# Kernel tuning notes

Hardware: AMD Instinct MI355X
Metric: run time of the kernel (lower is better)

The kernel has to match this reference:

```python
import jax, jax.numpy as jnp
import numpy as np

B, N, M, L, H = 32, 4096, 256, 128, 4
GAMMA = 2.0


def setup_inputs() -> dict:
    key = jax.random.key(0)
    kx, km, kv, ku, kw = jax.random.split(key, 5)
    x = jax.random.normal(kx, (B, N, M), dtype=jnp.float32)
    masks = (jax.random.uniform(km, (B, N)) > 0.3).astype(jnp.float32)
    # VarianceScaling(scale=0.1, fan_in, uniform) ~ small init; exact dist doesn't affect math
    V = jax.random.normal(kv, (H, M, L), dtype=jnp.float32) * 0.02
    U = jax.random.normal(ku, (H, M, L), dtype=jnp.float32) * 0.02
    w = jax.random.normal(kw, (H, L, 1), dtype=jnp.float32) * 0.05
    return {"x": x, "masks": masks, "V": V, "U": U, "w": w}


def reference(x, masks, V, U, w):
    # x: [B,N,M], masks: [B,N], V/U: [H,M,L], w: [H,L,1]
    m = masks[:, None, :, None]  # [B,1,N,1] broadcast over heads
    gated = jnp.tanh(jnp.einsum('bnm,hml->bhnl', x, V)) * jax.nn.sigmoid(
        jnp.einsum('bnm,hml->bhnl', x, U))          # [B,H,N,L]
    logits = jnp.einsum('bhnl,hl->bhn', gated, w[..., 0])[..., None]  # [B,H,N,1]
    a = m * logits                                   # masked logits (as in original)
    a = m * jnp.exp(a)                               # masked exp
    a = a / jnp.sum(a, axis=2, keepdims=True)        # softmax over instances
    ag = a ** GAMMA
    a = ag / jnp.sum(ag, axis=2, keepdims=True)      # gamma-power renorm
    emb = jnp.einsum('bhnk,bnm->bhm', a, x)          # weighted sum; k is the trailing 1
    emb = emb.reshape(B, H * M)                      # concat heads along axis=1
    att = jnp.transpose(a, (1, 0, 2, 3))             # [H,B,N,1] (per-head attention list)
    return (att, emb)
```

## Files before the change

### kernel.cpp

```cpp
#include <hip/hip_runtime.h>
#include <hip/hip_bf16.h>
#include <stdint.h>

#define B_ 32
#define N_ 4096
#define M_ 256
#define L_ 128
#define H_ 4
#define BN_ (B_ * N_)

typedef __bf16 bf16x8 __attribute__((ext_vector_type(8)));
typedef float  f32x4  __attribute__((ext_vector_type(4)));

__device__ __forceinline__ unsigned short f2bf(float f) {
    unsigned int u = __float_as_uint(f);
    u += 0x7fffu + ((u >> 16) & 1u);
    return (unsigned short)(u >> 16);
}
__device__ __forceinline__ unsigned int pack2(float lo, float hi) {
    return (unsigned int)f2bf(lo) | ((unsigned int)f2bf(hi) << 16);
}

__device__ __forceinline__ void gload16(const void* g, void* l) {
    __builtin_amdgcn_global_load_lds(
        (const __attribute__((address_space(1))) unsigned int*)g,
        (__attribute__((address_space(3))) unsigned int*)l, 16, 0, 0);
}


__global__ void prep_x(const float* __restrict__ x, unsigned short* __restrict__ xb) {
    const int blk  = blockIdx.x;
    const int tile = blk >> 2, ks = blk & 3;
    const int i    = threadIdx.x;
    const int kk   = (i & 7) * 8;
    const int tl   = kk >> 5;
    const int kl   = kk & 31;
    char* dst = (char*)xb + ((size_t)tile * 8 + ks * 2 + tl) * 8192;
#pragma unroll
    for (int rep = 0; rep < 4; ++rep) {
        int row = rep * 32 + (i >> 3);
        const float* gx = x + (size_t)(tile * 128 + row) * M_ + ks * 64 + kk;
        float4 a = *(const float4*)gx;
        float4 b = *(const float4*)(gx + 4);
        uint4 o;
        o.x = pack2(a.x, a.y); o.y = pack2(a.z, a.w);
        o.z = pack2(b.x, b.y); o.w = pack2(b.z, b.w);
        int byte = (row * 64 + kl * 2) ^ ((row & 6) << 3);
        *(uint4*)(dst + byte) = o;
    }
}

__global__ void prep_vu_img(const float* __restrict__ V, const float* __restrict__ U,
                            unsigned short* __restrict__ vu) {
    __shared__ float slab[64][129];
    const int b   = blockIdx.x;
    const int mat = b & 1, ks = (b >> 1) & 3, h = b >> 3;
    const float* src = (mat ? U : V) + ((size_t)h * M_ + ks * 64) * L_;
    const int tid = threadIdx.x;
#pragma unroll
    for (int rep = 0; rep < 32; ++rep) {
        int idx = rep * 256 + tid;
        slab[idx >> 7][idx & 127] = src[(size_t)(idx >> 7) * L_ + (idx & 127)];
    }
    __syncthreads();
#pragma unroll
    for (int rep = 0; rep < 4; ++rep) {
        int cidx = rep * 256 + tid;
        int l  = cidx >> 3;
        int kk = (cidx & 7) * 8;
        uint4 o;
        o.x = pack2(slab[kk + 0][l], slab[kk + 1][l]);
        o.y = pack2(slab[kk + 2][l], slab[kk + 3][l]);
        o.z = pack2(slab[kk + 4][l], slab[kk + 5][l]);
        o.w = pack2(slab[kk + 6][l], slab[kk + 7][l]);
        int tl = kk >> 5, kl = kk & 31;
        char* dst = (char*)vu + (((size_t)(h * 8 + ks * 2 + tl)) * 2 + mat) * 8192;
        int byte = (l * 64 + kl * 2) ^ ((l & 6) << 3);
        *(uint4*)(dst + byte) = o;
    }
}

__global__ __launch_bounds__(256, 2)
void gemm_fast3(const unsigned short* __restrict__ xb,
                const unsigned short* __restrict__ vu,
                const float* __restrict__ w,
                float* __restrict__ logits) {
    __shared__ __align__(16) unsigned short xs[3][4096];
    __shared__ __align__(16) unsigned short vs[3][4096];
    __shared__ __align__(16) unsigned short us[3][4096];

    const int orig    = blockIdx.x;
    const int logical = (orig & 7) * 512 + (orig >> 3);
    const int tile    = logical >> 2;
    const int h       = logical & 3;

    const int tid  = threadIdx.x;
    const int lane = tid & 63;
    const int wv   = tid >> 6;
    const int g    = lane >> 4;
    const int c    = lane & 15;

    f32x4 accV[2][8], accU[2][8];
#pragma unroll
    for (int rf = 0; rf < 2; ++rf)
#pragma unroll
        for (int cf = 0; cf < 8; ++cf) {
            accV[rf][cf] = (f32x4){0.f, 0.f, 0.f, 0.f};
            accU[rf][cf] = (f32x4){0.f, 0.f, 0.f, 0.f};
        }

    const int soff = wv * 2048;

    const char* gxs = (const char*)xb + (size_t)tile * 65536 + soff + lane * 16;
    const char* gvs = (const char*)vu + (size_t)h * 131072 + soff + lane * 16;
    const char* gus = gvs + 8192;

    int ar = wv * 32 + c;
    const int aoff0 = (ar * 64 + g * 16) ^ ((ar & 6) << 3);
    const int aoff1 = ((ar + 16) * 64 + g * 16) ^ (((ar + 16) & 6) << 3);
    int boff[8];
#pragma unroll
    for (int cf = 0; cf < 8; ++cf) {
        int l = cf * 16 + c;
        boff[cf] = (l * 64 + g * 16) ^ ((l & 6) << 3);
    }

#define STAGE(t, bufi) do {                                          \
        const char* _gx = gxs + (t) * 8192;                          \
        const char* _gv = gvs + (t) * 16384;                         \
        const char* _gu = gus + (t) * 16384;                         \
        gload16(_gx,        (char*)xs[bufi] + soff);                 \
        gload16(_gx + 1024, (char*)xs[bufi] + soff + 1024);          \
        gload16(_gv,        (char*)vs[bufi] + soff);                 \
        gload16(_gv + 1024, (char*)vs[bufi] + soff + 1024);          \
        gload16(_gu,        (char*)us[bufi] + soff);                 \
        gload16(_gu + 1024, (char*)us[bufi] + soff + 1024);          \
    } while (0)

    STAGE(0, 0);
    STAGE(1, 1);

#pragma unroll
    for (int t = 0; t < 8; ++t) {
        if (t < 7) asm volatile("s_waitcnt vmcnt(6)" ::: "memory");
        else       asm volatile("s_waitcnt vmcnt(0)" ::: "memory");
        __builtin_amdgcn_s_barrier();
        __builtin_amdgcn_sched_barrier(0);

        if (t < 6) STAGE(t + 2, (t + 2) % 3);

        const int buf = t % 3;
        const char* xbuf = (const char*)xs[buf];
        const char* vbuf = (const char*)vs[buf];
        const char* ubuf = (const char*)us[buf];

        bf16x8 a0 = *(const bf16x8*)(xbuf + aoff0);
        bf16x8 a1 = *(const bf16x8*)(xbuf + aoff1);
#pragma unroll
        for (int cf = 0; cf < 8; ++cf) {
            bf16x8 bv = *(const bf16x8*)(vbuf + boff[cf]);
            bf16x8 bu = *(const bf16x8*)(ubuf + boff[cf]);
            accV[0][cf] = __builtin_amdgcn_mfma_f32_16x16x32_bf16(a0, bv, accV[0][cf], 0, 0, 0);
            accV[1][cf] = __builtin_amdgcn_mfma_f32_16x16x32_bf16(a1, bv, accV[1][cf], 0, 0, 0);
            accU[0][cf] = __builtin_amdgcn_mfma_f32_16x16x32_bf16(a0, bu, accU[0][cf], 0, 0, 0);
            accU[1][cf] = __builtin_amdgcn_mfma_f32_16x16x32_bf16(a1, bu, accU[1][cf], 0, 0, 0);
        }
    }
#undef STAGE

    const float* wrow = w + h * L_;
#pragma unroll
    for (int rf = 0; rf < 2; ++rf) {
        float plog[4] = {0.f, 0.f, 0.f, 0.f};
#pragma unroll
        for (int cf = 0; cf < 8; ++cf) {
            float wvv = wrow[cf * 16 + c];
#pragma unroll
            for (int i = 0; i < 4; ++i) {
                float vv = accV[rf][cf][i];
                float uu = accU[rf][cf][i];
                vv = fminf(fmaxf(vv, -20.f), 20.f);
                float A = __expf(2.f * vv);
                float E = __expf(fminf(-uu, 30.f));
                float gg = __fdividef(A - 1.f, (A + 1.f) * (1.f + E));
                plog[i] += gg * wvv;
            }
        }
#pragma unroll
        for (int i = 0; i < 4; ++i) {
            float v = plog[i];
            v += __shfl_xor(v, 1);
            v += __shfl_xor(v, 2);
            v += __shfl_xor(v, 4);
            v += __shfl_xor(v, 8);
            if (c == 0) {
                int rowflat = tile * 128 + wv * 32 + rf * 16 + g * 4 + i;
                int b = rowflat >> 12;
                int n = rowflat & (N_ - 1);
                logits[((size_t)b * H_ + h) * N_ + n] = v;
            }
        }
    }
}

__global__ void prep_vu_slow(const float* __restrict__ V, const float* __restrict__ U,
                             unsigned short* __restrict__ Vt, unsigned short* __restrict__ Ut) {
    int idx = blockIdx.x * 256 + threadIdx.x;
    int m = idx & (M_ - 1);
    int l = (idx >> 8) & (L_ - 1);
    int h = idx >> 15;
    Vt[idx] = f2bf(V[((size_t)h * M_ + m) * L_ + l]);
    Ut[idx] = f2bf(U[((size_t)h * M_ + m) * L_ + l]);
}

#define BM 128
#define BK 64

__global__ __launch_bounds__(256, 2)
void gemm_logits(const float* __restrict__ x,
                 const unsigned short* __restrict__ Vt,
                 const unsigned short* __restrict__ Ut,
                 const float* __restrict__ w,
                 float* __restrict__ logits) {
    __shared__ __align__(16) unsigned short xs[BM * BK];
    __shared__ __align__(16) unsigned short vs[L_ * BK];
    __shared__ __align__(16) unsigned short us[L_ * BK];
    __shared__ float wl[L_];

    const int h    = blockIdx.x >> 10;
    const int tile = blockIdx.x & 1023;
    const int row0 = tile * BM;
    const int tid  = threadIdx.x;
    const int lane = tid & 63;
    const int wave = tid >> 6;

    if (tid < L_) wl[tid] = w[h * L_ + tid];

    f32x4 accV[2][8], accU[2][8];
#pragma unroll
    for (int rf = 0; rf < 2; ++rf)
#pragma unroll
        for (int cf = 0; cf < 8; ++cf) {
            accV[rf][cf] = (f32x4){0.f, 0.f, 0.f, 0.f};
            accU[rf][cf] = (f32x4){0.f, 0.f, 0.f, 0.f};
        }

    const unsigned short* Vh = Vt + (size_t)h * L_ * M_;
    const unsigned short* Uh = Ut + (size_t)h * L_ * M_;
    const int g = lane >> 4;
    const int c = lane & 15;

    for (int ks = 0; ks < 4; ++ks) {
        const int k0 = ks * BK;
        __syncthreads();
#pragma unroll
        for (int p = 0; p < 4; ++p) {
            int row = p * 32 + (tid >> 3);
            int kk  = (tid & 7) * 8;
            const float* gx = x + (size_t)(row0 + row) * M_ + k0 + kk;
            float4 a = *(const float4*)gx;
            float4 b = *(const float4*)(gx + 4);
            uint4 o;
            o.x = pack2(a.x, a.y); o.y = pack2(a.z, a.w);
            o.z = pack2(b.x, b.y); o.w = pack2(b.z, b.w);
            int byte = (row * BK + kk) * 2;
            byte ^= (row & 7) << 4;
            *(uint4*)((char*)xs + byte) = o;
        }
#pragma unroll
        for (int p = 0; p < 4; ++p) {
            int l  = p * 32 + (tid >> 3);
            int kk = (tid & 7) * 8;
            uint4 v = *(const uint4*)(Vh + (size_t)l * M_ + k0 + kk);
            uint4 u = *(const uint4*)(Uh + (size_t)l * M_ + k0 + kk);
            int byte = (l * BK + kk) * 2;
            byte ^= (l & 7) << 4;
            *(uint4*)((char*)vs + byte) = v;
            *(uint4*)((char*)us + byte) = u;
        }
        __syncthreads();
#pragma unroll
        for (int ksub = 0; ksub < 2; ++ksub) {
            bf16x8 afr[2];
#pragma unroll
            for (int rf = 0; rf < 2; ++rf) {
                int row = wave * 32 + rf * 16 + c;
                int byte = (row * BK + ksub * 32 + g * 8) * 2;
                byte ^= (row & 7) << 4;
                afr[rf] = *(const bf16x8*)((const char*)xs + byte);
            }
#pragma unroll
            for (int cf = 0; cf < 8; ++cf) {
                int l = cf * 16 + c;
                int byte = (l * BK + ksub * 32 + g * 8) * 2;
                byte ^= (l & 7) << 4;
                bf16x8 bv = *(const bf16x8*)((const char*)vs + byte);
                bf16x8 bu = *(const bf16x8*)((const char*)us + byte);
#pragma unroll
                for (int rf = 0; rf < 2; ++rf) {
                    accV[rf][cf] = __builtin_amdgcn_mfma_f32_16x16x32_bf16(afr[rf], bv, accV[rf][cf], 0, 0, 0);
                    accU[rf][cf] = __builtin_amdgcn_mfma_f32_16x16x32_bf16(afr[rf], bu, accU[rf][cf], 0, 0, 0);
                }
            }
        }
    }
#pragma unroll
    for (int rf = 0; rf < 2; ++rf) {
        float plog[4] = {0.f, 0.f, 0.f, 0.f};
#pragma unroll
        for (int cf = 0; cf < 8; ++cf) {
            float wvv = wl[cf * 16 + c];
#pragma unroll
            for (int i = 0; i < 4; ++i) {
                float vv = accV[rf][cf][i];
                float uu = accU[rf][cf][i];
                vv = fminf(fmaxf(vv, -20.f), 20.f);
                float e2v = __expf(2.f * vv);
                float t = __fdividef(e2v - 1.f, e2v + 1.f);
                float s = __fdividef(1.f, 1.f + __expf(-uu));
                plog[i] += t * s * wvv;
            }
        }
#pragma unroll
        for (int i = 0; i < 4; ++i) {
            float v = plog[i];
            v += __shfl_xor(v, 1);
            v += __shfl_xor(v, 2);
            v += __shfl_xor(v, 4);
            v += __shfl_xor(v, 8);
            if (c == 0) {
                int rowflat = row0 + wave * 32 + rf * 16 + g * 4 + i;
                int b = rowflat >> 12;
                int n = rowflat & (N_ - 1);
                logits[((size_t)b * H_ + h) * N_ + n] = v;
            }
        }
    }
}

__global__ __launch_bounds__(256)
void softmax_att(const float* __restrict__ logits, const float* __restrict__ masks,
                 float* __restrict__ att) {
    const int bh = blockIdx.x;
    const int b = bh >> 2, h = bh & 3;
    __shared__ float e2s[N_];
    __shared__ float red[4];
    const int tid = threadIdx.x;

    float sum = 0.f;
#pragma unroll
    for (int i = 0; i < N_ / 256; ++i) {
        int n = i * 256 + tid;
        float lg = logits[((size_t)b * H_ + h) * N_ + n];
        float mv = masks[(size_t)b * N_ + n];
        float e = mv * __expf(mv * lg);
        float e2 = e * e;
        e2s[n] = e2;
        sum += e2;
    }
#pragma unroll
    for (int off = 32; off >= 1; off >>= 1) sum += __shfl_xor(sum, off);
    if ((tid & 63) == 0) red[tid >> 6] = sum;
    __syncthreads();
    float S = red[0] + red[1] + red[2] + red[3];
    float inv = 1.f / S;
#pragma unroll
    for (int i = 0; i < N_ / 256; ++i) {
        int n = i * 256 + tid;
        att[((size_t)h * B_ + b) * N_ + n] = e2s[n] * inv;
    }
}

#define NCH 32
#define CHUNK (N_ / NCH)

__global__ __launch_bounds__(256)
void emb_partial(const float* __restrict__ x, const float* __restrict__ att,
                 float* __restrict__ part) {
    const int bc = blockIdx.x;
    const int b = bc >> 5, ch = bc & 31;
    __shared__ float as[H_][CHUNK];
    const int tid = threadIdx.x;

    for (int i = tid; i < H_ * CHUNK; i += 256) {
        int hh = i >> 7;
        int j  = i & (CHUNK - 1);
        as[hh][j] = att[((size_t)hh * B_ + b) * N_ + ch * CHUNK + j];
    }
    __syncthreads();

    float a0 = 0.f, a1 = 0.f, a2 = 0.f, a3 = 0.f;
    const float* xp = x + ((size_t)b * N_ + ch * CHUNK) * M_ + tid;
#pragma unroll 4
    for (int j = 0; j < CHUNK; ++j) {
        float xv = xp[(size_t)j * M_];
        a0 += as[0][j] * xv;
        a1 += as[1][j] * xv;
        a2 += as[2][j] * xv;
        a3 += as[3][j] * xv;
    }
    float* pp = part + (size_t)bc * H_ * M_ + tid;
    pp[0 * M_] = a0; pp[1 * M_] = a1; pp[2 * M_] = a2; pp[3 * M_] = a3;
}

__global__ __launch_bounds__(256)
void emb_reduce(const float* __restrict__ part, float* __restrict__ emb) {
    int idx = blockIdx.x * 256 + threadIdx.x;
    int b = idx >> 10;
    int r = idx & 1023;
    float s = 0.f;
#pragma unroll
    for (int ci = 0; ci < NCH; ++ci)
        s += part[((size_t)(b * NCH + ci)) * (H_ * M_) + r];
    emb[idx] = s;
}

extern "C" void kernel_launch(void* const* d_in, const int* in_sizes, int n_in,
                              void* d_out, int out_size, void* d_ws, size_t ws_size,
                              hipStream_t stream) {
    const float* x     = (const float*)d_in[0];
    const float* masks = (const float*)d_in[1];
    const float* V     = (const float*)d_in[2];
    const float* U     = (const float*)d_in[3];
    const float* w     = (const float*)d_in[4];

    float* att = (float*)d_out;
    float* emb = att + (size_t)H_ * B_ * N_;

    char* ws = (char*)d_ws;
    const size_t XB_BYTES  = (size_t)1024 * 8 * 8192;
    const size_t VU_BYTES  = (size_t)64 * 8192;
    const size_t LG_BYTES  = (size_t)B_ * H_ * N_ * 4;
    const size_t PT_BYTES  = (size_t)B_ * NCH * H_ * M_ * 4;
    const size_t NEED_FAST = XB_BYTES + VU_BYTES + LG_BYTES + PT_BYTES;

    float* logits;
    float* partp;

    if (ws_size >= NEED_FAST) {
        unsigned short* xb = (unsigned short*)ws;
        unsigned short* vu = (unsigned short*)(ws + XB_BYTES);
        logits = (float*)(ws + XB_BYTES + VU_BYTES);
        partp  = (float*)(ws + XB_BYTES + VU_BYTES + LG_BYTES);

        prep_x     <<<4096, 256, 0, stream>>>(x, xb);
        prep_vu_img<<<32,   256, 0, stream>>>(V, U, vu);
        gemm_fast3 <<<4096, 256, 0, stream>>>(xb, vu, w, logits);
    } else {
        unsigned short* Vt = (unsigned short*)ws;
        unsigned short* Ut = (unsigned short*)(ws + 262144);
        logits = (float*)(ws + 524288);
        partp  = (float*)(ws + 524288 + LG_BYTES);

        prep_vu_slow<<<512, 256, 0, stream>>>(V, U, Vt, Ut);
        gemm_logits <<<4096, 256, 0, stream>>>(x, Vt, Ut, w, logits);
    }

    softmax_att<<<B_ * H_,              256, 0, stream>>>(logits, masks, att);
    emb_partial<<<B_ * NCH,             256, 0, stream>>>(x, att, partp);
    emb_reduce <<<(B_ * H_ * M_) / 256, 256, 0, stream>>>(partp, emb);
}
```

Baseline: 176.7 us.

## Fuse x bf16 conversion into GEMM loading fp32 x directly into registers

```diff
diff --git a/kernel.cpp b/kernel.cpp
--- a/kernel.cpp
+++ b/kernel.cpp
@@ -25,29 +25,6 @@
     __builtin_amdgcn_global_load_lds(
         (const __attribute__((address_space(1))) unsigned int*)g,
         (__attribute__((address_space(3))) unsigned int*)l, 16, 0, 0);
-}
-
-
-__global__ void prep_x(const float* __restrict__ x, unsigned short* __restrict__ xb) {
-    const int blk  = blockIdx.x;
-    const int tile = blk >> 2, ks = blk & 3;
-    const int i    = threadIdx.x;
-    const int kk   = (i & 7) * 8;
-    const int tl   = kk >> 5;
-    const int kl   = kk & 31;
-    char* dst = (char*)xb + ((size_t)tile * 8 + ks * 2 + tl) * 8192;
-#pragma unroll
-    for (int rep = 0; rep < 4; ++rep) {
-        int row = rep * 32 + (i >> 3);
-        const float* gx = x + (size_t)(tile * 128 + row) * M_ + ks * 64 + kk;
-        float4 a = *(const float4*)gx;
-        float4 b = *(const float4*)(gx + 4);
-        uint4 o;
-        o.x = pack2(a.x, a.y); o.y = pack2(a.z, a.w);
-        o.z = pack2(b.x, b.y); o.w = pack2(b.z, b.w);
-        int byte = (row * 64 + kl * 2) ^ ((row & 6) << 3);
-        *(uint4*)(dst + byte) = o;
-    }
 }
 
 __global__ void prep_vu_img(const float* __restrict__ V, const float* __restrict__ U,
@@ -81,13 +58,13 @@
 }
 
 __global__ __launch_bounds__(256, 2)
-void gemm_fast3(const unsigned short* __restrict__ xb,
+void gemm_fast4(const float* __restrict__ x,
                 const unsigned short* __restrict__ vu,
                 const float* __restrict__ w,
                 float* __restrict__ logits) {
-    __shared__ __align__(16) unsigned short xs[3][4096];
     __shared__ __align__(16) unsigned short vs[3][4096];
     __shared__ __align__(16) unsigned short us[3][4096];
+    __shared__ float part[2][128];
 
     const int orig    = blockIdx.x;
     const int logical = (orig & 7) * 512 + (orig >> 3);
@@ -99,88 +76,145 @@
     const int wv   = tid >> 6;
     const int g    = lane >> 4;
     const int c    = lane & 15;
-
-    f32x4 accV[2][8], accU[2][8];
-#pragma unroll
-    for (int rf = 0; rf < 2; ++rf)
-#pragma unroll
-        for (int cf = 0; cf < 8; ++cf) {
+    const int r0   = (wv & 1) * 64;
+    const int l0   = (wv >> 1) * 64;
+
+    f32x4 accV[4][4], accU[4][4];
+#pragma unroll
+    for (int rf = 0; rf < 4; ++rf)
+#pragma unroll
+        for (int cf = 0; cf < 4; ++cf) {
             accV[rf][cf] = (f32x4){0.f, 0.f, 0.f, 0.f};
             accU[rf][cf] = (f32x4){0.f, 0.f, 0.f, 0.f};
         }
 
     const int soff = wv * 2048;
 
-    const char* gxs = (const char*)xb + (size_t)tile * 65536 + soff + lane * 16;
     const char* gvs = (const char*)vu + (size_t)h * 131072 + soff + lane * 16;
-    const char* gus = gvs + 8192;
-
-    int ar = wv * 32 + c;
-    const int aoff0 = (ar * 64 + g * 16) ^ ((ar & 6) << 3);
-    const int aoff1 = ((ar + 16) * 64 + g * 16) ^ (((ar + 16) & 6) << 3);
-    int boff[8];
-#pragma unroll
-    for (int cf = 0; cf < 8; ++cf) {
-        int l = cf * 16 + c;
+
+    const float* xp0 = x + ((size_t)tile * 128 + r0 +  0 + c) * M_ + g * 8;
+    const float* xp1 = xp0 + 16 * M_;
+    const float* xp2 = xp0 + 32 * M_;
+    const float* xp3 = xp0 + 48 * M_;
+
+    int boff[4];
+#pragma unroll
+    for (int cf = 0; cf < 4; ++cf) {
+        int l = l0 + cf * 16 + c;
         boff[cf] = (l * 64 + g * 16) ^ ((l & 6) << 3);
     }
 
-#define STAGE(t, bufi) do {                                          \
-        const char* _gx = gxs + (t) * 8192;                          \
-        const char* _gv = gvs + (t) * 16384;                         \
-        const char* _gu = gus + (t) * 16384;                         \
-        gload16(_gx,        (char*)xs[bufi] + soff);                 \
-        gload16(_gx + 1024, (char*)xs[bufi] + soff + 1024);          \
-        gload16(_gv,        (char*)vs[bufi] + soff);                 \
-        gload16(_gv + 1024, (char*)vs[bufi] + soff + 1024);          \
-        gload16(_gu,        (char*)us[bufi] + soff);                 \
-        gload16(_gu + 1024, (char*)us[bufi] + soff + 1024);          \
-    } while (0)
-
-    STAGE(0, 0);
-    STAGE(1, 1);
-
-#pragma unroll
-    for (int t = 0; t < 8; ++t) {
-        if (t < 7) asm volatile("s_waitcnt vmcnt(6)" ::: "memory");
-        else       asm volatile("s_waitcnt vmcnt(0)" ::: "memory");
-        __builtin_amdgcn_s_barrier();
-        __builtin_amdgcn_sched_barrier(0);
-
-        if (t < 6) STAGE(t + 2, (t + 2) % 3);
-
-        const int buf = t % 3;
-        const char* xbuf = (const char*)xs[buf];
-        const char* vbuf = (const char*)vs[buf];
-        const char* ubuf = (const char*)us[buf];
-
-        bf16x8 a0 = *(const bf16x8*)(xbuf + aoff0);
-        bf16x8 a1 = *(const bf16x8*)(xbuf + aoff1);
-#pragma unroll
-        for (int cf = 0; cf < 8; ++cf) {
-            bf16x8 bv = *(const bf16x8*)(vbuf + boff[cf]);
-            bf16x8 bu = *(const bf16x8*)(ubuf + boff[cf]);
-            accV[0][cf] = __builtin_amdgcn_mfma_f32_16x16x32_bf16(a0, bv, accV[0][cf], 0, 0, 0);
-            accV[1][cf] = __builtin_amdgcn_mfma_f32_16x16x32_bf16(a1, bv, accV[1][cf], 0, 0, 0);
-            accU[0][cf] = __builtin_amdgcn_mfma_f32_16x16x32_bf16(a0, bu, accU[0][cf], 0, 0, 0);
-            accU[1][cf] = __builtin_amdgcn_mfma_f32_16x16x32_bf16(a1, bu, accU[1][cf], 0, 0, 0);
-        }
-    }
-#undef STAGE
-
-    const float* wrow = w + h * L_;
-#pragma unroll
-    for (int rf = 0; rf < 2; ++rf) {
+    float4 xr[8];
+    bf16x8 fa0, fa1, fa2, fa3;
+
+#define LOADX(T) do {                                                     \
+        xr[0] = *(const float4*)(xp0 + (T) * 32);                         \
+        xr[1] = *(const float4*)(xp0 + (T) * 32 + 4);                     \
+        xr[2] = *(const float4*)(xp1 + (T) * 32);                         \
+        xr[3] = *(const float4*)(xp1 + (T) * 32 + 4);                     \
+        xr[4] = *(const float4*)(xp2 + (T) * 32);                         \
+        xr[5] = *(const float4*)(xp2 + (T) * 32 + 4);                     \
+        xr[6] = *(const float4*)(xp3 + (T) * 32);                         \
+        xr[7] = *(const float4*)(xp3 + (T) * 32 + 4);                     \
+    } while (0)
+
+#define PK(F, A, Bv) do {                                                 \
+        F[0] = (__bf16)(A).x; F[1] = (__bf16)(A).y;                       \
+        F[2] = (__bf16)(A).z; F[3] = (__bf16)(A).w;                       \
+        F[4] = (__bf16)(Bv).x; F[5] = (__bf16)(Bv).y;                     \
+        F[6] = (__bf16)(Bv).z; F[7] = (__bf16)(Bv).w;                     \
+    } while (0)
+
+#define PACK() do {                                                       \
+        PK(fa0, xr[0], xr[1]); PK(fa1, xr[2], xr[3]);                     \
+        PK(fa2, xr[4], xr[5]); PK(fa3, xr[6], xr[7]);                     \
+    } while (0)
+
+#define STAGEB(T, BI) do {                                                \
+        const char* _gv = gvs + (T) * 16384;                              \
+        const char* _gu = _gv + 8192;                                     \
+        gload16(_gv,        (char*)vs[BI] + soff);                        \
+        gload16(_gv + 1024, (char*)vs[BI] + soff + 1024);                 \
+        gload16(_gu,        (char*)us[BI] + soff);                        \
+        gload16(_gu + 1024, (char*)us[BI] + soff + 1024);                 \
+    } while (0)
+
+#define COMPUTE(BI) do {                                                  \
+        const char* _vb = (const char*)vs[BI];                            \
+        const char* _ub = (const char*)us[BI];                            \
+        _Pragma("unroll")                                                 \
+        for (int cf = 0; cf < 4; ++cf) {                                  \
+            bf16x8 bv = *(const bf16x8*)(_vb + boff[cf]);                 \
+            bf16x8 bu = *(const bf16x8*)(_ub + boff[cf]);                 \
+            accV[0][cf] = __builtin_amdgcn_mfma_f32_16x16x32_bf16(fa0, bv, accV[0][cf], 0, 0, 0); \
+            accV[1][cf] = __builtin_amdgcn_mfma_f32_16x16x32_bf16(fa1, bv, accV[1][cf], 0, 0, 0); \
+            accV[2][cf] = __builtin_amdgcn_mfma_f32_16x16x32_bf16(fa2, bv, accV[2][cf], 0, 0, 0); \
+            accV[3][cf] = __builtin_amdgcn_mfma_f32_16x16x32_bf16(fa3, bv, accV[3][cf], 0, 0, 0); \
+            accU[0][cf] = __builtin_amdgcn_mfma_f32_16x16x32_bf16(fa0, bu, accU[0][cf], 0, 0, 0); \
+            accU[1][cf] = __builtin_amdgcn_mfma_f32_16x16x32_bf16(fa1, bu, accU[1][cf], 0, 0, 0); \
+            accU[2][cf] = __builtin_amdgcn_mfma_f32_16x16x32_bf16(fa2, bu, accU[2][cf], 0, 0, 0); \
+            accU[3][cf] = __builtin_amdgcn_mfma_f32_16x16x32_bf16(fa3, bu, accU[3][cf], 0, 0, 0); \
+        }                                                                 \
+    } while (0)
+
+#define SCHED __builtin_amdgcn_sched_barrier(0)
+
+#define STEPF(T, BC, BN2) do {                                            \
+        asm volatile("s_waitcnt vmcnt(4)" ::: "memory");                  \
+        __builtin_amdgcn_s_barrier(); SCHED;                              \
+        PACK(); SCHED;                                                    \
+        LOADX((T) + 1); SCHED;                                            \
+        STAGEB((T) + 2, BN2); SCHED;                                      \
+        COMPUTE(BC);                                                      \
+    } while (0)
+
+    STAGEB(0, 0);
+    SCHED;
+    LOADX(0);
+    SCHED;
+    STAGEB(1, 1);
+    SCHED;
+
+    STEPF(0, 0, 2);
+    STEPF(1, 1, 0);
+    STEPF(2, 2, 1);
+    STEPF(3, 0, 2);
+    STEPF(4, 1, 0);
+    STEPF(5, 2, 1);
+    {
+        asm volatile("s_waitcnt vmcnt(4)" ::: "memory");
+        __builtin_amdgcn_s_barrier(); SCHED;
+        PACK(); SCHED;
+        LOADX(7); SCHED;
+        COMPUTE(0);
+    }
+    {
+        asm volatile("s_waitcnt vmcnt(0)" ::: "memory");
+        __builtin_amdgcn_s_barrier(); SCHED;
+        PACK(); SCHED;
+        COMPUTE(1);
+    }
+
+#undef STEPF
+#undef COMPUTE
+#undef STAGEB
+#undef PACK
+#undef PK
+#undef LOADX
+
+    const float* wrow = w + h * L_ + l0;
+#pragma unroll
+    for (int rf = 0; rf < 4; ++rf) {
         float plog[4] = {0.f, 0.f, 0.f, 0.f};
 #pragma unroll
-        for (int cf = 0; cf < 8; ++cf) {
+        for (int cf = 0; cf < 4; ++cf) {
             float wvv = wrow[cf * 16 + c];
 #pragma unroll
             for (int i = 0; i < 4; ++i) {
-                float vv = accV[rf][cf][i];
-                float uu = accU[rf][cf][i];
-                vv = fminf(fmaxf(vv, -20.f), 20.f);
-                float A = __expf(2.f * vv);
+                float vvv = accV[rf][cf][i];
+                float uu  = accU[rf][cf][i];
+                vvv = fminf(fmaxf(vvv, -20.f), 20.f);
+                float A = __expf(2.f * vvv);
                 float E = __expf(fminf(-uu, 30.f));
                 float gg = __fdividef(A - 1.f, (A + 1.f) * (1.f + E));
                 plog[i] += gg * wvv;
@@ -193,13 +227,17 @@
             v += __shfl_xor(v, 2);
             v += __shfl_xor(v, 4);
             v += __shfl_xor(v, 8);
-            if (c == 0) {
-                int rowflat = tile * 128 + wv * 32 + rf * 16 + g * 4 + i;
-                int b = rowflat >> 12;
-                int n = rowflat & (N_ - 1);
-                logits[((size_t)b * H_ + h) * N_ + n] = v;
-            }
-        }
+            if (c == 0)
+                part[wv >> 1][r0 + rf * 16 + g * 4 + i] = v;
+        }
+    }
+    __syncthreads();
+    if (tid < 128) {
+        float v = part[0][tid] + part[1][tid];
+        int rowflat = tile * 128 + tid;
+        int b = rowflat >> 12;
+        int n = rowflat & (N_ - 1);
+        logits[((size_t)b * H_ + h) * N_ + n] = v;
     }
 }
 
@@ -428,24 +466,21 @@
     float* emb = att + (size_t)H_ * B_ * N_;
 
     char* ws = (char*)d_ws;
-    const size_t XB_BYTES  = (size_t)1024 * 8 * 8192;
     const size_t VU_BYTES  = (size_t)64 * 8192;
     const size_t LG_BYTES  = (size_t)B_ * H_ * N_ * 4;
     const size_t PT_BYTES  = (size_t)B_ * NCH * H_ * M_ * 4;
-    const size_t NEED_FAST = XB_BYTES + VU_BYTES + LG_BYTES + PT_BYTES;
+    const size_t NEED_FAST = VU_BYTES + LG_BYTES + PT_BYTES;
 
     float* logits;
     float* partp;
 
     if (ws_size >= NEED_FAST) {
-        unsigned short* xb = (unsigned short*)ws;
-        unsigned short* vu = (unsigned short*)(ws + XB_BYTES);
-        logits = (float*)(ws + XB_BYTES + VU_BYTES);
-        partp  = (float*)(ws + XB_BYTES + VU_BYTES + LG_BYTES);
-
-        prep_x     <<<4096, 256, 0, stream>>>(x, xb);
-        prep_vu_img<<<32,   256, 0, stream>>>(V, U, vu);
-        gemm_fast3 <<<4096, 256, 0, stream>>>(xb, vu, w, logits);
+        unsigned short* vuimg = (unsigned short*)ws;
+        logits = (float*)(ws + VU_BYTES);
+        partp  = (float*)(ws + VU_BYTES + LG_BYTES);
+
+        prep_vu_img<<<32,   256, 0, stream>>>(V, U, vuimg);
+        gemm_fast4 <<<4096, 256, 0, stream>>>(x, vuimg, w, logits);
     } else {
         unsigned short* Vt = (unsigned short*)ws;
         unsigned short* Ut = (unsigned short*)(ws + 262144);
```

Measured after the change: 231.0 us. +30.8%, slower.
